# Kernel tuning notes

Measured on AMD Instinct MI355X. Metric: run time of the kernel, lower is better.

## Reference

```python
import jax, jax.numpy as jnp
import numpy as np

BATCH, SEQ, IN, HID = 256, 512, 64, 512


def _xavier(key, shape):
    fan_in, fan_out = shape[1], shape[0]
    limit = float(np.sqrt(6.0 / (fan_in + fan_out)))
    return jax.random.uniform(key, shape, jnp.float32, -limit, limit)


def setup_inputs() -> dict:
    key = jax.random.key(0)
    k1, k2, k3 = jax.random.split(key, 3)
    return {
        "x": jax.random.normal(k1, (BATCH, SEQ, IN), jnp.float32),
        "h0": jnp.zeros((BATCH, HID), jnp.float32),
        "W_ih": _xavier(k2, (HID, IN)),
        "W_hh": _xavier(k3, (HID, HID)),
        "b_ih": jnp.zeros((HID,), jnp.float32),
        "b_hh": jnp.zeros((HID,), jnp.float32),
    }


def reference(x, h0, W_ih, W_hh, b_ih, b_hh):
    # Precompute input projection for all timesteps at once: (B,S,H)
    x_proj = jnp.einsum('bsi,hi->bsh', x, W_ih) + b_ih + b_hh

    def step(h, xp_t):
        h_new = jnp.tanh(xp_t + h @ W_hh.T)  # (B,H)
        return h_new, h_new

    # scan over time axis; xs must be time-major
    h_n, _ = jax.lax.scan(step, h0, jnp.swapaxes(x_proj, 0, 1))
    last_step_features = h_n  # out[:, -1, :] equals final hidden state
    return (last_step_features, h_n)
```

## Files before the change

### kernel.cpp

```cpp
#include <hip/hip_runtime.h>
#include <stdint.h>

#define BATCH 256
#define SEQ   512
#define INDIM 64
#define HID   512

#define NREG   368
#define NLDS   (HID - NREG)
#define NREG_C (NREG / 8)
#define NLDS_C (NLDS / 8)
#define NGROUPS (SEQ / 8)

typedef _Float16 half2_t __attribute__((ext_vector_type(2)));

__device__ __forceinline__ float dot2f(uint32_t w, uint32_t h, float acc) {
    return __builtin_amdgcn_fdot2(__builtin_bit_cast(half2_t, w),
                                  __builtin_bit_cast(half2_t, h),
                                  acc, false);
}

__device__ __forceinline__ uint32_t pack2(float a, float b) {
    half2_t h;
    h[0] = (_Float16)a;
    h[1] = (_Float16)b;
    return __builtin_bit_cast(uint32_t, h);
}

struct SmemLayout {
    _Float16 wlds[NLDS_C * HID * 8];
    _Float16 hbuf[2][HID];
    _Float16 xbuf[2][8][INDIM];
};

__global__ __launch_bounds__(512, 2)
void rnn_persist_kernel(const float* __restrict__ x,
                        const float* __restrict__ h0,
                        const float* __restrict__ W_ih,
                        const float* __restrict__ W_hh,
                        const float* __restrict__ b_ih,
                        const float* __restrict__ b_hh,
                        float* __restrict__ out)
{
    __shared__ SmemLayout sm;
    const int tid = threadIdx.x;
    const int b   = blockIdx.x;

    const float* wrow = W_hh + (size_t)tid * HID;

    uint32_t wreg[NREG / 2];
    #pragma unroll
    for (int c = 0; c < NREG_C; ++c) {
        float4 a  = ((const float4*)wrow)[2 * c];
        float4 bb = ((const float4*)wrow)[2 * c + 1];
        wreg[4 * c + 0] = pack2(a.x, a.y);
        wreg[4 * c + 1] = pack2(a.z, a.w);
        wreg[4 * c + 2] = pack2(bb.x, bb.y);
        wreg[4 * c + 3] = pack2(bb.z, bb.w);
    }

    const float* wtail = wrow + NREG;
    #pragma unroll
    for (int c = 0; c < NLDS_C; ++c) {
        float4 a  = ((const float4*)wtail)[2 * c];
        float4 bb = ((const float4*)wtail)[2 * c + 1];
        uint4 wv;
        wv.x = pack2(a.x, a.y);
        wv.y = pack2(a.z, a.w);
        wv.z = pack2(bb.x, bb.y);
        wv.w = pack2(bb.z, bb.w);
        *(uint4*)&sm.wlds[(size_t)(c * HID + tid) * 8] = wv;
    }

    const float* irow = W_ih + (size_t)tid * INDIM;
    uint32_t wih[INDIM / 2];
    #pragma unroll
    for (int c = 0; c < 8; ++c) {
        float4 a  = ((const float4*)irow)[2 * c];
        float4 bb = ((const float4*)irow)[2 * c + 1];
        wih[4 * c + 0] = pack2(a.x, a.y);
        wih[4 * c + 1] = pack2(a.z, a.w);
        wih[4 * c + 2] = pack2(bb.x, bb.y);
        wih[4 * c + 3] = pack2(bb.z, bb.w);
    }

    const float bsum = b_ih[tid] + b_hh[tid];

    float hval = h0[(size_t)b * HID + tid];
    sm.hbuf[0][tid] = (_Float16)hval;

    {
        const int r = tid >> 6, c = tid & 63;
        float v = x[((size_t)b * SEQ + r) * INDIM + c];
        sm.xbuf[0][r][c] = (_Float16)v;
    }
    __syncthreads();

    float xnext = 0.0f;
    #pragma unroll 1
    for (int t = 0; t < SEQ; ++t) {
        const int g    = t >> 3;
        const int lt   = t & 7;
        const int p    = t & 1;
        const int slot = g & 1;

        if (lt == 0 && g + 1 < NGROUPS) {
            const int r = tid >> 6, c = tid & 63;
            xnext = x[((size_t)b * SEQ + (size_t)(g + 1) * 8 + r) * INDIM + c];
        }

        float acc = bsum;

        const uint4* xb4 = (const uint4*)&sm.xbuf[slot][lt][0];
        #pragma unroll
        for (int k = 0; k < 8; ++k) {
            uint4 xc = xb4[k];
            acc = dot2f(wih[4 * k + 0], xc.x, acc);
            acc = dot2f(wih[4 * k + 1], xc.y, acc);
            acc = dot2f(wih[4 * k + 2], xc.z, acc);
            acc = dot2f(wih[4 * k + 3], xc.w, acc);
        }

        const uint4* hb4 = (const uint4*)&sm.hbuf[p][0];

        #pragma unroll
        for (int c = 0; c < NREG_C; ++c) {
            uint4 hc = hb4[c];
            acc = dot2f(wreg[4 * c + 0], hc.x, acc);
            acc = dot2f(wreg[4 * c + 1], hc.y, acc);
            acc = dot2f(wreg[4 * c + 2], hc.z, acc);
            acc = dot2f(wreg[4 * c + 3], hc.w, acc);
        }

        #pragma unroll
        for (int c = 0; c < NLDS_C; ++c) {
            uint4 wc = *(const uint4*)&sm.wlds[(size_t)(c * HID + tid) * 8];
            uint4 hc = hb4[NREG_C + c];
            acc = dot2f(wc.x, hc.x, acc);
            acc = dot2f(wc.y, hc.y, acc);
            acc = dot2f(wc.z, hc.z, acc);
            acc = dot2f(wc.w, hc.w, acc);
        }

        float hnew = tanhf(acc);
        sm.hbuf[1 - p][tid] = (_Float16)hnew;

        if (lt == 5 && g + 1 < NGROUPS) {
            const int r = tid >> 6, c = tid & 63;
            sm.xbuf[(g + 1) & 1][r][c] = (_Float16)xnext;
        }

        __syncthreads();
        hval = hnew;
    }

    out[(size_t)b * HID + tid] = hval;
    out[(size_t)BATCH * HID + (size_t)b * HID + tid] = hval;
}

extern "C" void kernel_launch(void* const* d_in, const int* in_sizes, int n_in,
                              void* d_out, int out_size, void* d_ws, size_t ws_size,
                              hipStream_t stream) {
    (void)in_sizes; (void)n_in; (void)out_size; (void)d_ws; (void)ws_size;
    const float* x    = (const float*)d_in[0];
    const float* h0   = (const float*)d_in[1];
    const float* W_ih = (const float*)d_in[2];
    const float* W_hh = (const float*)d_in[3];
    const float* b_ih = (const float*)d_in[4];
    const float* b_hh = (const float*)d_in[5];
    float* out = (float*)d_out;

    hipLaunchKernelGGL(rnn_persist_kernel, dim3(BATCH), dim3(512), 0, stream,
                       x, h0, W_ih, W_hh, b_ih, b_hh, out);
}
```

Before: 1.145 ms.

## Split hidden-state dot products across 8-lane groups with DPP reduction

```diff
diff --git a/kernel.cpp b/kernel.cpp
--- a/kernel.cpp
+++ b/kernel.cpp
@@ -6,156 +6,162 @@
 #define INDIM 64
 #define HID   512
 
-#define NREG   368
-#define NLDS   (HID - NREG)
-#define NREG_C (NREG / 8)
-#define NLDS_C (NLDS / 8)
-#define NGROUPS (SEQ / 8)
-
 typedef _Float16 half2_t __attribute__((ext_vector_type(2)));
 
 __device__ __forceinline__ float dot2f(uint32_t w, uint32_t h, float acc) {
     return __builtin_amdgcn_fdot2(__builtin_bit_cast(half2_t, w),
-                                  __builtin_bit_cast(half2_t, h),
-                                  acc, false);
+                                  __builtin_bit_cast(half2_t, h), acc, false);
+}
+__device__ __forceinline__ uint32_t pack2(float a, float b) {
+    half2_t h; h[0] = (_Float16)a; h[1] = (_Float16)b;
+    return __builtin_bit_cast(uint32_t, h);
+}
+template<int CTRL>
+__device__ __forceinline__ float dpp_sum(float x) {
+    int xi = __builtin_bit_cast(int, x);
+    int yi = __builtin_amdgcn_mov_dpp(xi, CTRL, 0xF, 0xF, true);
+    return x + __builtin_bit_cast(float, yi);
+}
+__device__ __forceinline__ float swz4_sum(float x) {
+    int xi = __builtin_bit_cast(int, x);
+    int yi = __builtin_amdgcn_ds_swizzle(xi, 0x101F);
+    return x + __builtin_bit_cast(float, yi);
 }
 
-__device__ __forceinline__ uint32_t pack2(float a, float b) {
-    half2_t h;
-    h[0] = (_Float16)a;
-    h[1] = (_Float16)b;
-    return __builtin_bit_cast(uint32_t, h);
-}
-
-struct SmemLayout {
-    _Float16 wlds[NLDS_C * HID * 8];
-    _Float16 hbuf[2][HID];
-    _Float16 xbuf[2][8][INDIM];
+struct Smem {
+    uint4     wl[16][512];
+    _Float16  hbuf[2][8][72];
 };
 
+#define DOT4(accv, wrow, hc) \
+    accv = dot2f((wrow)[0], hc.x, accv); accv = dot2f((wrow)[1], hc.y, accv); \
+    accv = dot2f((wrow)[2], hc.z, accv); accv = dot2f((wrow)[3], hc.w, accv);
+
 __global__ __launch_bounds__(512, 2)
-void rnn_persist_kernel(const float* __restrict__ x,
-                        const float* __restrict__ h0,
-                        const float* __restrict__ W_ih,
-                        const float* __restrict__ W_hh,
-                        const float* __restrict__ b_ih,
-                        const float* __restrict__ b_hh,
-                        float* __restrict__ out)
+void rnn_ksplit_kernel(const float* __restrict__ x,
+                       const float* __restrict__ h0,
+                       const float* __restrict__ W_ih,
+                       const float* __restrict__ W_hh,
+                       const float* __restrict__ b_ih,
+                       const float* __restrict__ b_hh,
+                       float* __restrict__ out)
 {
-    __shared__ SmemLayout sm;
-    const int tid = threadIdx.x;
-    const int b   = blockIdx.x;
+    __shared__ Smem sm;
+    const int t = threadIdx.x;
+    const int b = blockIdx.x;
+    const int s = t & 7;
+    const int rbase = t & ~7;
 
-    const float* wrow = W_hh + (size_t)tid * HID;
-
-    uint32_t wreg[NREG / 2];
+    uint32_t wreg[6][32];
     #pragma unroll
-    for (int c = 0; c < NREG_C; ++c) {
-        float4 a  = ((const float4*)wrow)[2 * c];
-        float4 bb = ((const float4*)wrow)[2 * c + 1];
-        wreg[4 * c + 0] = pack2(a.x, a.y);
-        wreg[4 * c + 1] = pack2(a.z, a.w);
-        wreg[4 * c + 2] = pack2(bb.x, bb.y);
-        wreg[4 * c + 3] = pack2(bb.z, bb.w);
+    for (int j = 0; j < 6; ++j) {
+        const float* wr = W_hh + (size_t)(rbase + j) * HID + s * 64;
+        #pragma unroll
+        for (int q = 0; q < 16; ++q) {
+            float4 v4 = ((const float4*)wr)[q];
+            wreg[j][2*q]   = pack2(v4.x, v4.y);
+            wreg[j][2*q+1] = pack2(v4.z, v4.w);
+        }
+    }
+    #pragma unroll
+    for (int v = 0; v < 2; ++v) {
+        const float* wr = W_hh + (size_t)(rbase + 6 + v) * HID + s * 64;
+        #pragma unroll
+        for (int c = 0; c < 8; ++c) {
+            float4 aa = ((const float4*)wr)[2*c];
+            float4 bb = ((const float4*)wr)[2*c+1];
+            uint4 wv;
+            wv.x = pack2(aa.x, aa.y); wv.y = pack2(aa.z, aa.w);
+            wv.z = pack2(bb.x, bb.y); wv.w = pack2(bb.z, bb.w);
+            sm.wl[v*8 + c][t] = wv;
+        }
+    }
+    uint32_t wih[8][4];
+    #pragma unroll
+    for (int j = 0; j < 8; ++j) {
+        const float* wr = W_ih + (size_t)(rbase + j) * INDIM + s * 8;
+        float4 aa = ((const float4*)wr)[0];
+        float4 bb = ((const float4*)wr)[1];
+        wih[j][0] = pack2(aa.x, aa.y); wih[j][1] = pack2(aa.z, aa.w);
+        wih[j][2] = pack2(bb.x, bb.y); wih[j][3] = pack2(bb.z, bb.w);
     }
 
-    const float* wtail = wrow + NREG;
-    #pragma unroll
-    for (int c = 0; c < NLDS_C; ++c) {
-        float4 a  = ((const float4*)wtail)[2 * c];
-        float4 bb = ((const float4*)wtail)[2 * c + 1];
-        uint4 wv;
-        wv.x = pack2(a.x, a.y);
-        wv.y = pack2(a.z, a.w);
-        wv.z = pack2(bb.x, bb.y);
-        wv.w = pack2(bb.z, bb.w);
-        *(uint4*)&sm.wlds[(size_t)(c * HID + tid) * 8] = wv;
+    const float bsum = b_ih[t] + b_hh[t];
+    sm.hbuf[0][t >> 6][t & 63] = (_Float16)h0[(size_t)b * HID + t];
+
+    const float* xbase = x + (size_t)b * SEQ * INDIM + s * 8;
+    float4 xa = ((const float4*)xbase)[0];
+    float4 xb = ((const float4*)xbase)[1];
+
+    const bool b0 = (s & 1) != 0, b1 = (s & 2) != 0, b2 = (s & 4) != 0;
+
+    __syncthreads();
+
+    float hlast = 0.f;
+    #pragma unroll 1
+    for (int tt = 0; tt < SEQ; ++tt) {
+        const int tn = (tt + 1 < SEQ) ? tt + 1 : tt;
+        const float* xp = xbase + (size_t)tn * INDIM;
+        float4 xa_n = ((const float4*)xp)[0];
+        float4 xb_n = ((const float4*)xp)[1];
+
+        const int par = tt & 1;
+        float a0=0,a1=0,a2=0,a3=0,a4=0,a5=0,a6=0,a7=0;
+        const uint4* hp = (const uint4*)&sm.hbuf[par][s][0];
+
+        #pragma unroll
+        for (int c = 0; c < 8; ++c) {
+            uint4 hc = hp[c];
+            uint4 w6 = sm.wl[c][t];
+            uint4 w7 = sm.wl[8 + c][t];
+            DOT4(a0, &wreg[0][4*c], hc);
+            DOT4(a1, &wreg[1][4*c], hc);
+            DOT4(a2, &wreg[2][4*c], hc);
+            DOT4(a3, &wreg[3][4*c], hc);
+            DOT4(a4, &wreg[4][4*c], hc);
+            DOT4(a5, &wreg[5][4*c], hc);
+            a6 = dot2f(w6.x, hc.x, a6); a6 = dot2f(w6.y, hc.y, a6);
+            a6 = dot2f(w6.z, hc.z, a6); a6 = dot2f(w6.w, hc.w, a6);
+            a7 = dot2f(w7.x, hc.x, a7); a7 = dot2f(w7.y, hc.y, a7);
+            a7 = dot2f(w7.z, hc.z, a7); a7 = dot2f(w7.w, hc.w, a7);
+        }
+
+        {
+            uint32_t xp0 = pack2(xa.x, xa.y), xp1 = pack2(xa.z, xa.w);
+            uint32_t xp2 = pack2(xb.x, xb.y), xp3 = pack2(xb.z, xb.w);
+            uint4 xc; xc.x = xp0; xc.y = xp1; xc.z = xp2; xc.w = xp3;
+            DOT4(a0, wih[0], xc); DOT4(a1, wih[1], xc);
+            DOT4(a2, wih[2], xc); DOT4(a3, wih[3], xc);
+            DOT4(a4, wih[4], xc); DOT4(a5, wih[5], xc);
+            DOT4(a6, wih[6], xc); DOT4(a7, wih[7], xc);
+        }
+
+        float t0 = dpp_sum<0xB1>(a0), u0 = dpp_sum<0xB1>(a1);
+        float t1 = dpp_sum<0xB1>(a2), u1 = dpp_sum<0xB1>(a3);
+        float t2 = dpp_sum<0xB1>(a4), u2 = dpp_sum<0xB1>(a5);
+        float t3 = dpp_sum<0xB1>(a6), u3 = dpp_sum<0xB1>(a7);
+        float q0 = b0 ? u0 : t0;
+        float q1 = b0 ? u1 : t1;
+        float q2 = b0 ? u2 : t2;
+        float q3 = b0 ? u3 : t3;
+        float r0a = dpp_sum<0x4E>(q0), r0b = dpp_sum<0x4E>(q1);
+        float r1a = dpp_sum<0x4E>(q2), r1b = dpp_sum<0x4E>(q3);
+        float r0 = b1 ? r0b : r0a;
+        float r1 = b1 ? r1b : r1a;
+        float f0 = swz4_sum(r0), f1 = swz4_sum(r1);
+        float acc = (b2 ? f1 : f0) + bsum;
+
+        float e  = __expf(2.0f * acc);
+        float th = 1.0f - 2.0f * __builtin_amdgcn_rcpf(e + 1.0f);
+
+        sm.hbuf[1 - par][t >> 6][t & 63] = (_Float16)th;
+        hlast = th;
+        xa = xa_n; xb = xb_n;
+        __syncthreads();
     }
 
-    const float* irow = W_ih + (size_t)tid * INDIM;
-    uint32_t wih[INDIM / 2];
-    #pragma unroll
-    for (int c = 0; c < 8; ++c) {
-        float4 a  = ((const float4*)irow)[2 * c];
-        float4 bb = ((const float4*)irow)[2 * c + 1];
-        wih[4 * c + 0] = pack2(a.x, a.y);
-        wih[4 * c + 1] = pack2(a.z, a.w);
-        wih[4 * c + 2] = pack2(bb.x, bb.y);
-        wih[4 * c + 3] = pack2(bb.z, bb.w);
-    }
-
-    const float bsum = b_ih[tid] + b_hh[tid];
-
-    float hval = h0[(size_t)b * HID + tid];
-    sm.hbuf[0][tid] = (_Float16)hval;
-
-    {
-        const int r = tid >> 6, c = tid & 63;
-        float v = x[((size_t)b * SEQ + r) * INDIM + c];
-        sm.xbuf[0][r][c] = (_Float16)v;
-    }
-    __syncthreads();
-
-    float xnext = 0.0f;
-    #pragma unroll 1
-    for (int t = 0; t < SEQ; ++t) {
-        const int g    = t >> 3;
-        const int lt   = t & 7;
-        const int p    = t & 1;
-        const int slot = g & 1;
-
-        if (lt == 0 && g + 1 < NGROUPS) {
-            const int r = tid >> 6, c = tid & 63;
-            xnext = x[((size_t)b * SEQ + (size_t)(g + 1) * 8 + r) * INDIM + c];
-        }
-
-        float acc = bsum;
-
-        const uint4* xb4 = (const uint4*)&sm.xbuf[slot][lt][0];
-        #pragma unroll
-        for (int k = 0; k < 8; ++k) {
-            uint4 xc = xb4[k];
-            acc = dot2f(wih[4 * k + 0], xc.x, acc);
-            acc = dot2f(wih[4 * k + 1], xc.y, acc);
-            acc = dot2f(wih[4 * k + 2], xc.z, acc);
-            acc = dot2f(wih[4 * k + 3], xc.w, acc);
-        }
-
-        const uint4* hb4 = (const uint4*)&sm.hbuf[p][0];
-
-        #pragma unroll
-        for (int c = 0; c < NREG_C; ++c) {
-            uint4 hc = hb4[c];
-            acc = dot2f(wreg[4 * c + 0], hc.x, acc);
-            acc = dot2f(wreg[4 * c + 1], hc.y, acc);
-            acc = dot2f(wreg[4 * c + 2], hc.z, acc);
-            acc = dot2f(wreg[4 * c + 3], hc.w, acc);
-        }
-
-        #pragma unroll
-        for (int c = 0; c < NLDS_C; ++c) {
-            uint4 wc = *(const uint4*)&sm.wlds[(size_t)(c * HID + tid) * 8];
-            uint4 hc = hb4[NREG_C + c];
-            acc = dot2f(wc.x, hc.x, acc);
-            acc = dot2f(wc.y, hc.y, acc);
-            acc = dot2f(wc.z, hc.z, acc);
-            acc = dot2f(wc.w, hc.w, acc);
-        }
-
-        float hnew = tanhf(acc);
-        sm.hbuf[1 - p][tid] = (_Float16)hnew;
-
-        if (lt == 5 && g + 1 < NGROUPS) {
-            const int r = tid >> 6, c = tid & 63;
-            sm.xbuf[(g + 1) & 1][r][c] = (_Float16)xnext;
-        }
-
-        __syncthreads();
-        hval = hnew;
-    }
-
-    out[(size_t)b * HID + tid] = hval;
-    out[(size_t)BATCH * HID + (size_t)b * HID + tid] = hval;
+    out[(size_t)b * HID + t] = hlast;
+    out[(size_t)BATCH * HID + (size_t)b * HID + t] = hlast;
 }
 
 extern "C" void kernel_launch(void* const* d_in, const int* in_sizes, int n_in,
@@ -170,6 +176,6 @@
     const float* b_hh = (const float*)d_in[5];
     float* out = (float*)d_out;
 
-    hipLaunchKernelGGL(rnn_persist_kernel, dim3(BATCH), dim3(512), 0, stream,
+    hipLaunchKernelGGL(rnn_ksplit_kernel, dim3(BATCH), dim3(512), 0, stream,
                        x, h0, W_ih, W_hh, b_ih, b_hh, out);
 }
```

Result: faster. 962.3 us (-15.9%).
